# Kernel optimization log

Hardware: AMD Instinct MI355X
Metric: run time of the kernel (lower is better)

## Reference

```python
import jax, jax.numpy as jnp
import numpy as np

EMB = 512
N_ROWS = 10000
N_PAIRS = 65536


def setup_inputs() -> dict:
    key = jax.random.key(0)
    ks = jax.random.split(key, 10)
    s1 = 1.0 / np.sqrt(2 * EMB)
    s2 = 1.0 / np.sqrt(128)
    s3 = 1.0 / np.sqrt(64)
    return {
        "pos_pairs": jax.random.randint(ks[0], (N_PAIRS, 3), 0, N_ROWS, dtype=jnp.int32),
        "neg_pairs": jax.random.randint(ks[1], (N_PAIRS, 3), 0, N_ROWS, dtype=jnp.int32),
        "drug_embedding": jax.random.normal(ks[2], (N_ROWS, EMB), dtype=jnp.float32),
        "target_embedding": jax.random.normal(ks[3], (N_ROWS, EMB), dtype=jnp.float32),
        "W1": jax.random.normal(ks[4], (2 * EMB, 128), dtype=jnp.float32) * s1,
        "b1": jnp.zeros((128,), dtype=jnp.float32),
        "W2": jax.random.normal(ks[5], (128, 64), dtype=jnp.float32) * s2,
        "b2": jnp.zeros((64,), dtype=jnp.float32),
        "W3": jax.random.normal(ks[6], (64, 1), dtype=jnp.float32) * s3,
        "b3": jnp.zeros((1,), dtype=jnp.float32),
    }


def _mlp(x, W1, b1, W2, b2, W3, b3):
    h = jax.nn.relu(x @ W1 + b1)
    h = jax.nn.relu(h @ W2 + b2)
    return (h @ W3 + b3)[..., 0]  # [N]


def _pair_loss(pairs, drug_emb, tgt_emb, W1, b1, W2, b2, W3, b3):
    d = drug_emb[pairs[:, 0]]            # [N, EMB]
    t1 = tgt_emb[pairs[:, 1]]            # [N, EMB]
    t2 = tgt_emb[pairs[:, 2]]            # [N, EMB]
    a1 = _mlp(jnp.concatenate([d, t1], axis=-1), W1, b1, W2, b2, W3, b3)
    a2 = _mlp(jnp.concatenate([d, t2], axis=-1), W1, b1, W2, b2, W3, b3)
    # per-pair MSE of scalar affinities = (a1 - a2)^2; mean over pairs
    return jnp.mean((a1 - a2) ** 2)


def reference(pos_pairs, neg_pairs, drug_embedding, target_embedding,
              W1, b1, W2, b2, W3, b3):
    pos = _pair_loss(pos_pairs, drug_embedding, target_embedding, W1, b1, W2, b2, W3, b3)
    neg = _pair_loss(neg_pairs, drug_embedding, target_embedding, W1, b1, W2, b2, W3, b3)
    return pos - neg
```

## Files before the change

### kernel.cpp

```cpp
#include <hip/hip_runtime.h>

#define EMB 512
#define NROWS 10000
#define NPAIRS 65536

typedef __bf16 bf16x8 __attribute__((ext_vector_type(8)));
typedef float  f32x4  __attribute__((ext_vector_type(4)));
typedef unsigned int u32x4 __attribute__((ext_vector_type(4)));

__device__ __forceinline__ void split2(float x0, float x1, unsigned* hw, unsigned* lw) {
    unsigned u0 = __float_as_uint(x0), u1 = __float_as_uint(x1);
    unsigned r0 = u0 + 0x7FFFu + ((u0 >> 16) & 1u);
    unsigned r1 = u1 + 0x7FFFu + ((u1 >> 16) & 1u);
    float h0 = __uint_as_float(r0 & 0xFFFF0000u);
    float h1 = __uint_as_float(r1 & 0xFFFF0000u);
    float l0 = x0 - h0, l1 = x1 - h1;
    unsigned v0 = __float_as_uint(l0), v1 = __float_as_uint(l1);
    unsigned s0 = v0 + 0x7FFFu + ((v0 >> 16) & 1u);
    unsigned s1 = v1 + 0x7FFFu + ((v1 >> 16) & 1u);
    *hw = (r0 >> 16) | (r1 & 0xFFFF0000u);
    *lw = (s0 >> 16) | (s1 & 0xFFFF0000u);
}

__global__ __launch_bounds__(256)
void k0_fragment(const float* __restrict__ W1, const float* __restrict__ W2,
                 unsigned short* __restrict__ W1Fhi, unsigned short* __restrict__ W1Flo,
                 unsigned short* __restrict__ W2Fhi, unsigned short* __restrict__ W2Flo)
{
    int e = blockIdx.x * 256 + threadIdx.x;
    float x;
    unsigned short *hp, *lp;
    if (e < 131072) {
        int i  = e & 7;
        int l  = (e >> 3) & 63;
        int nt = (e >> 9) & 7;
        int kt = (e >> 12) & 15;
        int t  = e >> 16;
        int k = kt * 32 + 8 * (l >> 4) + i;
        int n = nt * 16 + (l & 15);
        x = W1[(t * 512 + k) * 128 + n];
        hp = W1Fhi + e; lp = W1Flo + e;
    } else {
        int e2 = e - 131072;
        int i  = e2 & 7;
        int l  = (e2 >> 3) & 63;
        int nt = (e2 >> 9) & 3;
        int kt = e2 >> 11;
        int k = kt * 32 + 8 * (l >> 4) + i;
        int n = nt * 16 + (l & 15);
        x = W2[k * 64 + n];
        hp = W2Fhi + e2; lp = W2Flo + e2;
    }
    unsigned u = __float_as_uint(x);
    unsigned r = u + 0x7FFFu + ((u >> 16) & 1u);
    float hf = __uint_as_float(r & 0xFFFF0000u);
    float lf = x - hf;
    unsigned v = __float_as_uint(lf);
    unsigned s = v + 0x7FFFu + ((v >> 16) & 1u);
    *hp = (unsigned short)(r >> 16);
    *lp = (unsigned short)(s >> 16);
}

#define K1_RPB 79
#define K1_NCH 5

__global__ __launch_bounds__(256, 2)
void k1_mfma(const float* __restrict__ drug, const float* __restrict__ tgt,
             const unsigned* __restrict__ W1Fhi, const unsigned* __restrict__ W1Flo,
             const float* __restrict__ b1,
             float* __restrict__ D, float* __restrict__ T)
{
    __shared__ unsigned short Ah[2][16][512];
    __shared__ unsigned short Al[2][16][512];

    int bid = blockIdx.x, tid = threadIdx.x;
    int t  = bid & 1;
    int ch = (bid >> 1) & 1;
    int rg = bid >> 2;
    const float* emb = t ? tgt : drug;
    float* out = t ? T : D;
    int row_base = rg * K1_RPB;

    int wave = tid >> 6, lane = tid & 63;
    int g = lane >> 4, lm = lane & 15;
    int nt = ch * 4 + wave;

    const u32x4* BH = (const u32x4*)W1Fhi + (t ? 8192 : 0);
    const u32x4* BL = (const u32x4*)W1Flo + (t ? 8192 : 0);

    u32x4 bhv[16], blv[16];
    #pragma unroll
    for (int kt = 0; kt < 16; kt++) {
        bhv[kt] = BH[(kt * 8 + nt) * 64 + lane];
        blv[kt] = BL[(kt * 8 + nt) * 64 + lane];
    }
    float bias = t ? 0.f : b1[nt * 16 + lm];

    float4 va[4][2];
    #pragma unroll
    for (int i = 0; i < 4; i++) {
        int gr = row_base + 0 * 16 + wave * 4 + i;
        if (gr > NROWS - 1) gr = NROWS - 1;
        const float* src = emb + (size_t)gr * EMB + lane * 8;
        va[i][0] = *(const float4*)src;
        va[i][1] = *(const float4*)(src + 4);
    }

    #pragma unroll
    for (int c = 0; c < K1_NCH; c++) {
        float4 vb[4][2];
        if (c + 1 < K1_NCH) {
            #pragma unroll
            for (int i = 0; i < 4; i++) {
                int gr = row_base + (c + 1) * 16 + wave * 4 + i;
                if (gr > NROWS - 1) gr = NROWS - 1;
                const float* src = emb + (size_t)gr * EMB + lane * 8;
                vb[i][0] = *(const float4*)src;
                vb[i][1] = *(const float4*)(src + 4);
            }
        }
        #pragma unroll
        for (int i = 0; i < 4; i++) {
            int lr = wave * 4 + i;
            unsigned h0, h1, h2, h3, l0, l1, l2, l3;
            split2(va[i][0].x, va[i][0].y, &h0, &l0);
            split2(va[i][0].z, va[i][0].w, &h1, &l1);
            split2(va[i][1].x, va[i][1].y, &h2, &l2);
            split2(va[i][1].z, va[i][1].w, &h3, &l3);
            u32x4 hq, lq;
            hq[0]=h0; hq[1]=h1; hq[2]=h2; hq[3]=h3;
            lq[0]=l0; lq[1]=l1; lq[2]=l2; lq[3]=l3;
            int cc = lane ^ (lr & 7);
            *(u32x4*)((char*)&Ah[c & 1][0][0] + lr * 1024 + cc * 16) = hq;
            *(u32x4*)((char*)&Al[c & 1][0][0] + lr * 1024 + cc * 16) = lq;
        }
        __syncthreads();
        f32x4 acc;
        acc[0]=0.f; acc[1]=0.f; acc[2]=0.f; acc[3]=0.f;
        #pragma unroll
        for (int kt = 0; kt < 16; kt++) {
            int cc = (kt * 4 + g) ^ (lm & 7);
            u32x4 ahq = *(const u32x4*)((const char*)&Ah[c & 1][0][0] + lm * 1024 + cc * 16);
            u32x4 alq = *(const u32x4*)((const char*)&Al[c & 1][0][0] + lm * 1024 + cc * 16);
            bf16x8 Af = __builtin_bit_cast(bf16x8, ahq);
            bf16x8 Alf = __builtin_bit_cast(bf16x8, alq);
            bf16x8 Bh = __builtin_bit_cast(bf16x8, bhv[kt]);
            bf16x8 Bl = __builtin_bit_cast(bf16x8, blv[kt]);
            acc = __builtin_amdgcn_mfma_f32_16x16x32_bf16(Af, Bh, acc, 0, 0, 0);
            acc = __builtin_amdgcn_mfma_f32_16x16x32_bf16(Af, Bl, acc, 0, 0, 0);
            acc = __builtin_amdgcn_mfma_f32_16x16x32_bf16(Alf, Bh, acc, 0, 0, 0);
        }
        #pragma unroll
        for (int reg = 0; reg < 4; reg++) {
            int lr = c * 16 + 4 * g + reg;
            int row = row_base + lr;
            if (lr < K1_RPB && row < NROWS)
                out[row * 128 + nt * 16 + lm] = acc[reg] + bias;
        }
        #pragma unroll
        for (int i = 0; i < 4; i++) { va[i][0] = vb[i][0]; va[i][1] = vb[i][1]; }
    }
}

__global__ __launch_bounds__(256)
void k2_pairs(const float* __restrict__ D, const float* __restrict__ T,
              const int* __restrict__ pos, const int* __restrict__ neg,
              const unsigned* __restrict__ W2Fhi, const unsigned* __restrict__ W2Flo,
              const float* __restrict__ b2, const float* __restrict__ W3,
              double* __restrict__ partials)
{
    __shared__ u32x4 Ash[4][768];

    int tid = threadIdx.x;
    int wave = tid >> 6, lane = tid & 63;
    int g = lane >> 4, lm = lane & 15;
    int rr = lane >> 3, cc = lane & 7;
    int gw = blockIdx.x * 4 + wave;
    const int* pairs = (gw < 2048) ? pos : neg;
    int p0 = (gw & 2047) * 32;

    const float* bp[12];
    #pragma unroll
    for (int it = 0; it < 12; it++) {
        int pr = it * 8 + rr;
        int idxv;
        const float* src;
        if (pr < 32) { idxv = pairs[(p0 + pr) * 3]; src = D; }
        else { int q = pr - 32; idxv = pairs[(p0 + (q >> 1)) * 3 + 1 + (q & 1)]; src = T; }
        bp[it] = src + (size_t)idxv * 128 + ((cc ^ (pr & 7)) << 2);
    }

    u32x4* A4w = &Ash[wave][0];
    const u32x4* BH4 = (const u32x4*)W2Fhi;
    const u32x4* BL4 = (const u32x4*)W2Flo;

    f32x4 acc[4][4];
    #pragma unroll
    for (int mt = 0; mt < 4; mt++)
        #pragma unroll
        for (int nt = 0; nt < 4; nt++) { acc[mt][nt][0]=0.f; acc[mt][nt][1]=0.f; acc[mt][nt][2]=0.f; acc[mt][nt][3]=0.f; }

    #pragma unroll 1
    for (int kt = 0; kt < 4; kt++) {
        u32x4 bh[4], bl[4];
        #pragma unroll
        for (int nt = 0; nt < 4; nt++) {
            bh[nt] = BH4[(kt * 4 + nt) * 64 + lane];
            bl[nt] = BL4[(kt * 4 + nt) * 64 + lane];
        }
        #pragma unroll
        for (int it = 0; it < 12; it++) {
            __builtin_amdgcn_global_load_lds(
                (const __attribute__((address_space(1))) void*)(bp[it] + kt * 32),
                (__attribute__((address_space(3))) void*)((char*)A4w + it * 1024),
                16, 0, 0);
        }
        asm volatile("s_waitcnt vmcnt(0)" ::: "memory");
        #pragma unroll
        for (int mt = 0; mt < 4; mt++) {
            int r = mt * 16 + lm;
            int p = r >> 1;
            int ds = p & 7, ts = r & 7;
            const f32x4* drow = (const f32x4*)(A4w + p * 8);
            const f32x4* trow = (const f32x4*)(A4w + (32 + r) * 8);
            f32x4 d0 = drow[(2 * g) ^ ds];
            f32x4 d1 = drow[(2 * g + 1) ^ ds];
            f32x4 t0 = trow[(2 * g) ^ ts];
            f32x4 t1 = trow[(2 * g + 1) ^ ts];
            float h0 = fmaxf(d0[0] + t0[0], 0.f), h1v = fmaxf(d0[1] + t0[1], 0.f);
            float h2 = fmaxf(d0[2] + t0[2], 0.f), h3 = fmaxf(d0[3] + t0[3], 0.f);
            float h4 = fmaxf(d1[0] + t1[0], 0.f), h5 = fmaxf(d1[1] + t1[1], 0.f);
            float h6 = fmaxf(d1[2] + t1[2], 0.f), h7 = fmaxf(d1[3] + t1[3], 0.f);
            unsigned hq0, hq1, hq2, hq3, lq0, lq1, lq2, lq3;
            split2(h0, h1v, &hq0, &lq0);
            split2(h2, h3,  &hq1, &lq1);
            split2(h4, h5,  &hq2, &lq2);
            split2(h6, h7,  &hq3, &lq3);
            u32x4 ah, al;
            ah[0]=hq0; ah[1]=hq1; ah[2]=hq2; ah[3]=hq3;
            al[0]=lq0; al[1]=lq1; al[2]=lq2; al[3]=lq3;
            bf16x8 Ahf = __builtin_bit_cast(bf16x8, ah);
            bf16x8 Alf = __builtin_bit_cast(bf16x8, al);
            #pragma unroll
            for (int nt = 0; nt < 4; nt++) {
                bf16x8 Bh = __builtin_bit_cast(bf16x8, bh[nt]);
                bf16x8 Bl = __builtin_bit_cast(bf16x8, bl[nt]);
                acc[mt][nt] = __builtin_amdgcn_mfma_f32_16x16x32_bf16(Ahf, Bh, acc[mt][nt], 0, 0, 0);
                acc[mt][nt] = __builtin_amdgcn_mfma_f32_16x16x32_bf16(Ahf, Bl, acc[mt][nt], 0, 0, 0);
                acc[mt][nt] = __builtin_amdgcn_mfma_f32_16x16x32_bf16(Alf, Bh, acc[mt][nt], 0, 0, 0);
            }
        }
        asm volatile("s_waitcnt lgkmcnt(0)" ::: "memory");
    }

    float b2v[4], w3v[4];
    #pragma unroll
    for (int nt = 0; nt < 4; nt++) { b2v[nt] = b2[nt * 16 + lm]; w3v[nt] = W3[nt * 16 + lm]; }

    float pr[4][4];
    #pragma unroll
    for (int mt = 0; mt < 4; mt++)
        #pragma unroll
        for (int reg = 0; reg < 4; reg++) {
            float s = 0.f;
            #pragma unroll
            for (int nt = 0; nt < 4; nt++) {
                float h2 = fmaxf(acc[mt][nt][reg] + b2v[nt], 0.f);
                s = fmaf(h2, w3v[nt], s);
            }
            pr[mt][reg] = s;
        }
    #pragma unroll
    for (int m = 1; m <= 8; m <<= 1)
        #pragma unroll
        for (int mt = 0; mt < 4; mt++)
            #pragma unroll
            for (int reg = 0; reg < 4; reg++)
                pr[mt][reg] += __shfl_xor(pr[mt][reg], m, 64);

    double dsq = 0.0;
    #pragma unroll
    for (int mt = 0; mt < 4; mt++) {
        float d0 = pr[mt][0] - pr[mt][1];
        float d1 = pr[mt][2] - pr[mt][3];
        dsq += (double)d0 * (double)d0 + (double)d1 * (double)d1;
    }
    dsq += __shfl_xor(dsq, 16, 64);
    dsq += __shfl_xor(dsq, 32, 64);

    __syncthreads();
    if (lane == 0) ((double*)&Ash[wave][0])[0] = dsq;
    __syncthreads();
    if (tid == 0) {
        double sum = 0.0;
        #pragma unroll
        for (int w = 0; w < 4; w++) sum += ((double*)&Ash[w][0])[0];
        partials[blockIdx.x] = sum;
    }
}

__global__ void k3_final(const double* __restrict__ partials, float* __restrict__ out)
{
    int lane = threadIdx.x;
    double sp = 0.0, sn = 0.0;
    #pragma unroll
    for (int i = 0; i < 8; i++) {
        sp += partials[lane + 64 * i];
        sn += partials[512 + lane + 64 * i];
    }
    #pragma unroll
    for (int m = 1; m <= 32; m <<= 1) {
        sp += __shfl_xor(sp, m, 64);
        sn += __shfl_xor(sn, m, 64);
    }
    if (lane == 0) out[0] = (float)((sp - sn) / (double)NPAIRS);
}

extern "C" void kernel_launch(void* const* d_in, const int* in_sizes, int n_in,
                              void* d_out, int out_size, void* d_ws, size_t ws_size,
                              hipStream_t stream) {
    const int*   pos  = (const int*)d_in[0];
    const int*   neg  = (const int*)d_in[1];
    const float* drug = (const float*)d_in[2];
    const float* tgt  = (const float*)d_in[3];
    const float* W1   = (const float*)d_in[4];
    const float* b1   = (const float*)d_in[5];
    const float* W2   = (const float*)d_in[6];
    const float* b2   = (const float*)d_in[7];
    const float* W3   = (const float*)d_in[8];

    float* Dp = (float*)d_ws;
    float* Tp = Dp + NROWS * 128;
    char* base = (char*)(Tp + NROWS * 128);
    unsigned short* W2Fhi = (unsigned short*)base;
    unsigned short* W2Flo = W2Fhi + 8192;
    unsigned short* W1Fhi = W2Flo + 8192;
    unsigned short* W1Flo = W1Fhi + 131072;
    double* partials = (double*)(W1Flo + 131072);
    float* out = (float*)d_out;

    k0_fragment<<<544, 256, 0, stream>>>(W1, W2, W1Fhi, W1Flo, W2Fhi, W2Flo);
    k1_mfma<<<512, 256, 0, stream>>>(drug, tgt, (const unsigned*)W1Fhi,
                                     (const unsigned*)W1Flo, b1, Dp, Tp);
    k2_pairs<<<1024, 256, 0, stream>>>(Dp, Tp, pos, neg, (const unsigned*)W2Fhi,
                                       (const unsigned*)W2Flo, b2, W3, partials);
    k3_final<<<1, 64, 0, stream>>>(partials, out);
}
```

Baseline: 58.03 us.

## Pre-split embeddings to bf16 hi/lo in a separate pass before streaming GEMM

Adds a kernel that converts both embedding tables into bf16 hi/lo halves in workspace. A new k1_stream kernel then feeds MFMA straight from these pre-split arrays without LDS staging or in-kernel conversion. The path is taken only when the workspace is large enough. In exchange it adds an extra pass that reads the full fp32 tables and writes the same number of bytes back, plus one more kernel launch, and k1_stream runs only 250 blocks with no load prefetch.

```diff
diff --git a/kernel.cpp b/kernel.cpp
--- a/kernel.cpp
+++ b/kernel.cpp
@@ -61,6 +61,82 @@
     *lp = (unsigned short)(s >> 16);
 }
 
+__global__ __launch_bounds__(256)
+void k0b_split(const float* __restrict__ drug, const float* __restrict__ tgt,
+               unsigned short* __restrict__ EHi, unsigned short* __restrict__ ELo)
+{
+    int e = blockIdx.x * 256 + threadIdx.x;
+    const float* src;
+    int off;
+    if (e < 1280000) { src = drug; off = e; }
+    else             { src = tgt;  off = e - 1280000; }
+    float4 v = ((const float4*)src)[off];
+    unsigned h01, l01, h23, l23;
+    split2(v.x, v.y, &h01, &l01);
+    split2(v.z, v.w, &h23, &l23);
+    *(uint2*)(EHi + (size_t)e * 4) = make_uint2(h01, h23);
+    *(uint2*)(ELo + (size_t)e * 4) = make_uint2(l01, l23);
+}
+
+__global__ __launch_bounds__(512, 2)
+void k1_stream(const unsigned* __restrict__ EHi, const unsigned* __restrict__ ELo,
+               const unsigned* __restrict__ W1Fhi, const unsigned* __restrict__ W1Flo,
+               const float* __restrict__ b1,
+               float* __restrict__ D, float* __restrict__ T)
+{
+    int bid = blockIdx.x, tid = threadIdx.x;
+    bool isT = bid >= 125;
+    int rg = isT ? bid - 125 : bid;
+    float* out = isT ? T : D;
+    int row0 = rg * 80;
+
+    int wave = tid >> 6, lane = tid & 63;
+    int g = lane >> 4, lm = lane & 15;
+    int nt = wave;
+
+    const u32x4* BH = (const u32x4*)W1Fhi + (isT ? 8192 : 0);
+    const u32x4* BL = (const u32x4*)W1Flo + (isT ? 8192 : 0);
+    const u32x4* AH = (const u32x4*)EHi + (isT ? (size_t)NROWS * 64 : 0);
+    const u32x4* AL = (const u32x4*)ELo + (isT ? (size_t)NROWS * 64 : 0);
+
+    u32x4 bhv[16], blv[16];
+    #pragma unroll
+    for (int kt = 0; kt < 16; kt++) {
+        bhv[kt] = BH[(kt * 8 + nt) * 64 + lane];
+        blv[kt] = BL[(kt * 8 + nt) * 64 + lane];
+    }
+    float bias = isT ? 0.f : b1[nt * 16 + lm];
+
+    #pragma unroll 1
+    for (int c = 0; c < 5; c++) {
+        int row = row0 + c * 16 + lm;
+        const u32x4* ah = AH + (size_t)row * 64;
+        const u32x4* al = AL + (size_t)row * 64;
+
+        f32x4 acc;
+        acc[0] = 0.f; acc[1] = 0.f; acc[2] = 0.f; acc[3] = 0.f;
+
+        #pragma unroll
+        for (int kt = 0; kt < 16; kt++) {
+            u32x4 ahq = ah[kt * 4 + g];
+            u32x4 alq = al[kt * 4 + g];
+            bf16x8 Ah = __builtin_bit_cast(bf16x8, ahq);
+            bf16x8 Al = __builtin_bit_cast(bf16x8, alq);
+            bf16x8 Bh = __builtin_bit_cast(bf16x8, bhv[kt]);
+            bf16x8 Bl = __builtin_bit_cast(bf16x8, blv[kt]);
+            acc = __builtin_amdgcn_mfma_f32_16x16x32_bf16(Ah, Bh, acc, 0, 0, 0);
+            acc = __builtin_amdgcn_mfma_f32_16x16x32_bf16(Ah, Bl, acc, 0, 0, 0);
+            acc = __builtin_amdgcn_mfma_f32_16x16x32_bf16(Al, Bh, acc, 0, 0, 0);
+        }
+
+        #pragma unroll
+        for (int reg = 0; reg < 4; reg++) {
+            int r = row0 + c * 16 + 4 * g + reg;
+            out[r * 128 + nt * 16 + lm] = acc[reg] + bias;
+        }
+    }
+}
+
 #define K1_RPB 79
 #define K1_NCH 5
 
@@ -99,7 +175,7 @@
     float4 va[4][2];
     #pragma unroll
     for (int i = 0; i < 4; i++) {
-        int gr = row_base + 0 * 16 + wave * 4 + i;
+        int gr = row_base + wave * 4 + i;
         if (gr > NROWS - 1) gr = NROWS - 1;
         const float* src = emb + (size_t)gr * EMB + lane * 8;
         va[i][0] = *(const float4*)src;
@@ -337,11 +413,23 @@
     unsigned short* W1Fhi = W2Flo + 8192;
     unsigned short* W1Flo = W1Fhi + 131072;
     double* partials = (double*)(W1Flo + 131072);
+    unsigned short* EHi = (unsigned short*)(partials + 1024);
+    unsigned short* ELo = EHi + 2 * NROWS * EMB;
     float* out = (float*)d_out;
 
+    size_t need = (size_t)((char*)(ELo + 2 * NROWS * EMB) - (char*)d_ws);
+    bool presplit = ws_size >= need;
+
     k0_fragment<<<544, 256, 0, stream>>>(W1, W2, W1Fhi, W1Flo, W2Fhi, W2Flo);
-    k1_mfma<<<512, 256, 0, stream>>>(drug, tgt, (const unsigned*)W1Fhi,
-                                     (const unsigned*)W1Flo, b1, Dp, Tp);
+    if (presplit) {
+        k0b_split<<<10000, 256, 0, stream>>>(drug, tgt, EHi, ELo);
+        k1_stream<<<250, 512, 0, stream>>>((const unsigned*)EHi, (const unsigned*)ELo,
+                                           (const unsigned*)W1Fhi, (const unsigned*)W1Flo,
+                                           b1, Dp, Tp);
+    } else {
+        k1_mfma<<<512, 256, 0, stream>>>(drug, tgt, (const unsigned*)W1Fhi,
+                                         (const unsigned*)W1Flo, b1, Dp, Tp);
+    }
     k2_pairs<<<1024, 256, 0, stream>>>(Dp, Tp, pos, neg, (const unsigned*)W2Fhi,
                                        (const unsigned*)W2Flo, b2, W3, partials);
     k3_final<<<1, 64, 0, stream>>>(partials, out);
```

Result: slower. 92.34 us (+59.1%).

## Double-buffer LDS gathers in pair kernel and halve pairs per wave

Applied to the files above, without the earlier changes.

The pair kernel now handles 16 pairs per wave instead of 32, so it launches twice as many blocks, and the final reduction reads twice as many partials. The LDS staging buffer is split into two halves. The next k-slice's gathered rows and W2 fragments are prefetched while the current slice's MFMAs run, using a partial vmcnt wait. This aims to hide gather latency and raise occupancy. In exchange, each wave does less MFMA work per launch, and the hand-written waitcnt counts must match the number of outstanding loads.

```diff
diff --git a/kernel.cpp b/kernel.cpp
--- a/kernel.cpp
+++ b/kernel.cpp
@@ -99,7 +99,7 @@
     float4 va[4][2];
     #pragma unroll
     for (int i = 0; i < 4; i++) {
-        int gr = row_base + 0 * 16 + wave * 4 + i;
+        int gr = row_base + wave * 4 + i;
         if (gr > NROWS - 1) gr = NROWS - 1;
         const float* src = emb + (size_t)gr * EMB + lane * 8;
         va[i][0] = *(const float4*)src;
@@ -169,60 +169,77 @@
               const float* __restrict__ b2, const float* __restrict__ W3,
               double* __restrict__ partials)
 {
-    __shared__ u32x4 Ash[4][768];
+    __shared__ u32x4 Ash[4][2][384];
 
     int tid = threadIdx.x;
     int wave = tid >> 6, lane = tid & 63;
     int g = lane >> 4, lm = lane & 15;
     int rr = lane >> 3, cc = lane & 7;
     int gw = blockIdx.x * 4 + wave;
-    const int* pairs = (gw < 2048) ? pos : neg;
-    int p0 = (gw & 2047) * 32;
-
-    const float* bp[12];
-    #pragma unroll
-    for (int it = 0; it < 12; it++) {
+    const int* pairs = (gw < 4096) ? pos : neg;
+    int p0 = (gw & 4095) * 16;
+
+    const float* bp[6];
+    #pragma unroll
+    for (int it = 0; it < 6; it++) {
         int pr = it * 8 + rr;
         int idxv;
         const float* src;
-        if (pr < 32) { idxv = pairs[(p0 + pr) * 3]; src = D; }
-        else { int q = pr - 32; idxv = pairs[(p0 + (q >> 1)) * 3 + 1 + (q & 1)]; src = T; }
+        if (pr < 16) { idxv = pairs[(p0 + pr) * 3]; src = D; }
+        else { int q = pr - 16; idxv = pairs[(p0 + (q >> 1)) * 3 + 1 + (q & 1)]; src = T; }
         bp[it] = src + (size_t)idxv * 128 + ((cc ^ (pr & 7)) << 2);
     }
 
-    u32x4* A4w = &Ash[wave][0];
     const u32x4* BH4 = (const u32x4*)W2Fhi;
     const u32x4* BL4 = (const u32x4*)W2Flo;
 
-    f32x4 acc[4][4];
-    #pragma unroll
-    for (int mt = 0; mt < 4; mt++)
+    f32x4 acc[2][4];
+    #pragma unroll
+    for (int mt = 0; mt < 2; mt++)
         #pragma unroll
         for (int nt = 0; nt < 4; nt++) { acc[mt][nt][0]=0.f; acc[mt][nt][1]=0.f; acc[mt][nt][2]=0.f; acc[mt][nt][3]=0.f; }
 
-    #pragma unroll 1
+    u32x4 bhc[4], blc[4];
+    #pragma unroll
+    for (int nt = 0; nt < 4; nt++) {
+        bhc[nt] = BH4[(0 * 4 + nt) * 64 + lane];
+        blc[nt] = BL4[(0 * 4 + nt) * 64 + lane];
+    }
+    #pragma unroll
+    for (int it = 0; it < 6; it++)
+        __builtin_amdgcn_global_load_lds(
+            (const __attribute__((address_space(1))) void*)(bp[it]),
+            (__attribute__((address_space(3))) void*)((char*)&Ash[wave][0][0] + it * 1024),
+            16, 0, 0);
+
+    #pragma unroll
     for (int kt = 0; kt < 4; kt++) {
-        u32x4 bh[4], bl[4];
-        #pragma unroll
-        for (int nt = 0; nt < 4; nt++) {
-            bh[nt] = BH4[(kt * 4 + nt) * 64 + lane];
-            bl[nt] = BL4[(kt * 4 + nt) * 64 + lane];
-        }
-        #pragma unroll
-        for (int it = 0; it < 12; it++) {
-            __builtin_amdgcn_global_load_lds(
-                (const __attribute__((address_space(1))) void*)(bp[it] + kt * 32),
-                (__attribute__((address_space(3))) void*)((char*)A4w + it * 1024),
-                16, 0, 0);
-        }
-        asm volatile("s_waitcnt vmcnt(0)" ::: "memory");
-        #pragma unroll
-        for (int mt = 0; mt < 4; mt++) {
+        u32x4 bhn[4], bln[4];
+        if (kt < 3) {
+            #pragma unroll
+            for (int nt = 0; nt < 4; nt++) {
+                bhn[nt] = BH4[((kt + 1) * 4 + nt) * 64 + lane];
+                bln[nt] = BL4[((kt + 1) * 4 + nt) * 64 + lane];
+            }
+            asm volatile("s_waitcnt lgkmcnt(0)" ::: "memory");
+            #pragma unroll
+            for (int it = 0; it < 6; it++)
+                __builtin_amdgcn_global_load_lds(
+                    (const __attribute__((address_space(1))) void*)(bp[it] + (kt + 1) * 32),
+                    (__attribute__((address_space(3))) void*)((char*)&Ash[wave][(kt + 1) & 1][0] + it * 1024),
+                    16, 0, 0);
+            asm volatile("s_waitcnt vmcnt(14)" ::: "memory");
+        } else {
+            asm volatile("s_waitcnt vmcnt(0)" ::: "memory");
+        }
+        const u32x4* A4w = &Ash[wave][kt & 1][0];
+        #pragma unroll
+        for (int mt = 0; mt < 2; mt++) {
             int r = mt * 16 + lm;
             int p = r >> 1;
             int ds = p & 7, ts = r & 7;
             const f32x4* drow = (const f32x4*)(A4w + p * 8);
-            const f32x4* trow = (const f32x4*)(A4w + (32 + r) * 8);
+            const f32x4* trow = (const f32x4*)(A4w + (16 + r) * 8);
             f32x4 d0 = drow[(2 * g) ^ ds];
             f32x4 d1 = drow[(2 * g + 1) ^ ds];
             f32x4 t0 = trow[(2 * g) ^ ts];
@@ -243,23 +260,24 @@
             bf16x8 Alf = __builtin_bit_cast(bf16x8, al);
             #pragma unroll
             for (int nt = 0; nt < 4; nt++) {
-                bf16x8 Bh = __builtin_bit_cast(bf16x8, bh[nt]);
-                bf16x8 Bl = __builtin_bit_cast(bf16x8, bl[nt]);
+                bf16x8 Bh = __builtin_bit_cast(bf16x8, bhc[nt]);
+                bf16x8 Bl = __builtin_bit_cast(bf16x8, blc[nt]);
                 acc[mt][nt] = __builtin_amdgcn_mfma_f32_16x16x32_bf16(Ahf, Bh, acc[mt][nt], 0, 0, 0);
                 acc[mt][nt] = __builtin_amdgcn_mfma_f32_16x16x32_bf16(Ahf, Bl, acc[mt][nt], 0, 0, 0);
                 acc[mt][nt] = __builtin_amdgcn_mfma_f32_16x16x32_bf16(Alf, Bh, acc[mt][nt], 0, 0, 0);
             }
         }
-        asm volatile("s_waitcnt lgkmcnt(0)" ::: "memory");
+        #pragma unroll
+        for (int nt = 0; nt < 4; nt++) { bhc[nt] = bhn[nt]; blc[nt] = bln[nt]; }
     }
 
     float b2v[4], w3v[4];
     #pragma unroll
     for (int nt = 0; nt < 4; nt++) { b2v[nt] = b2[nt * 16 + lm]; w3v[nt] = W3[nt * 16 + lm]; }
 
-    float pr[4][4];
-    #pragma unroll
-    for (int mt = 0; mt < 4; mt++)
+    float pr[2][4];
+    #pragma unroll
+    for (int mt = 0; mt < 2; mt++)
         #pragma unroll
         for (int reg = 0; reg < 4; reg++) {
             float s = 0.f;
@@ -273,14 +291,14 @@
     #pragma unroll
     for (int m = 1; m <= 8; m <<= 1)
         #pragma unroll
-        for (int mt = 0; mt < 4; mt++)
+        for (int mt = 0; mt < 2; mt++)
             #pragma unroll
             for (int reg = 0; reg < 4; reg++)
                 pr[mt][reg] += __shfl_xor(pr[mt][reg], m, 64);
 
     double dsq = 0.0;
     #pragma unroll
-    for (int mt = 0; mt < 4; mt++) {
+    for (int mt = 0; mt < 2; mt++) {
         float d0 = pr[mt][0] - pr[mt][1];
         float d1 = pr[mt][2] - pr[mt][3];
         dsq += (double)d0 * (double)d0 + (double)d1 * (double)d1;
@@ -289,12 +307,12 @@
     dsq += __shfl_xor(dsq, 32, 64);
 
     __syncthreads();
-    if (lane == 0) ((double*)&Ash[wave][0])[0] = dsq;
+    if (lane == 0) ((double*)&Ash[wave][0][0])[0] = dsq;
     __syncthreads();
     if (tid == 0) {
         double sum = 0.0;
         #pragma unroll
-        for (int w = 0; w < 4; w++) sum += ((double*)&Ash[w][0])[0];
+        for (int w = 0; w < 4; w++) sum += ((double*)&Ash[w][0][0])[0];
         partials[blockIdx.x] = sum;
     }
 }
@@ -304,9 +322,9 @@
     int lane = threadIdx.x;
     double sp = 0.0, sn = 0.0;
     #pragma unroll
-    for (int i = 0; i < 8; i++) {
+    for (int i = 0; i < 16; i++) {
         sp += partials[lane + 64 * i];
-        sn += partials[512 + lane + 64 * i];
+        sn += partials[1024 + lane + 64 * i];
     }
     #pragma unroll
     for (int m = 1; m <= 32; m <<= 1) {
@@ -342,7 +360,7 @@
     k0_fragment<<<544, 256, 0, stream>>>(W1, W2, W1Fhi, W1Flo, W2Fhi, W2Flo);
     k1_mfma<<<512, 256, 0, stream>>>(drug, tgt, (const unsigned*)W1Fhi,
                                      (const unsigned*)W1Flo, b1, Dp, Tp);
-    k2_pairs<<<1024, 256, 0, stream>>>(Dp, Tp, pos, neg, (const unsigned*)W2Fhi,
+    k2_pairs<<<2048, 256, 0, stream>>>(Dp, Tp, pos, neg, (const unsigned*)W2Fhi,
                                        (const unsigned*)W2Flo, b2, W3, partials);
     k3_final<<<1, 64, 0, stream>>>(partials, out);
 }
```

New measurement: 55.73 us (median of 2 runs). -4.0%, faster.
